# Performance work log

Measured on AMD Instinct MI355X. Metric: run time of the kernel, lower is better.

## Reference

```python
import jax, jax.numpy as jnp
import numpy as np

NEG_SLOPE = 0.2


def gatv2(x, src, dst, eattr, Wl, bl, Wr, br, We, att, bias, concat):
    # GATv2Conv (PyG semantics): message j->i, softmax over incoming edges of target i.
    n = x.shape[0]
    H, C = att.shape
    xl = (x @ Wl + bl).reshape(n, H, C)   # source transform lin_l
    xr = (x @ Wr + br).reshape(n, H, C)   # target transform lin_r
    xe = (eattr @ We).reshape(-1, H, C)   # edge transform lin_edge (no bias)
    g = jax.nn.leaky_relu(xl[src] + xr[dst] + xe, NEG_SLOPE)  # [E,H,C]
    e = jnp.einsum('ehc,hc->eh', g, att)                      # [E,H]
    m = jax.ops.segment_max(e, dst, num_segments=n)
    a = jnp.exp(e - m[dst])
    s = jax.ops.segment_sum(a, dst, num_segments=n)
    alpha = a / (s[dst] + 1e-16)                              # [E,H]
    out = jax.ops.segment_sum(alpha[:, :, None] * xl[src], dst, num_segments=n)
    out = out.reshape(n, H * C) if concat else out.mean(axis=1)
    return out + bias, alpha


def add_self_loops(src, dst, eattr, n):
    # PyG default: add_self_loops=True, fill_value='mean' for edge_attr
    loop = jnp.arange(n, dtype=src.dtype)
    fill = jnp.broadcast_to(eattr.mean(axis=0, keepdims=True), (n, eattr.shape[1]))
    return (jnp.concatenate([src, loop]), jnp.concatenate([dst, loop]),
            jnp.concatenate([eattr, fill], axis=0))


def setup_inputs() -> dict:
    key = jax.random.key(0)
    ks = iter(jax.random.split(key, 64))
    B, N, D = 4, 2048, 256
    n = B * N
    E = 131072
    H, C1 = 4, 64  # conv1: heads=4, out=hidden//heads=64 (concat -> 256)
    C2 = 256       # conv2: heads=4, out=256, concat=False (mean)
    IN1 = 770

    def rn(shape, s=0.05):
        return jax.random.normal(next(ks), shape, dtype=jnp.float32) * s

    inp = {
        'h': rn((B, N, D), 1.0), 'c_temp': rn((B, N, D), 1.0),
        'c_stereo': rn((B, N, D), 1.0), 'e_proj': rn((B, N, 2), 1.0),
        'f_Lt': rn((B, N, D), 1.0),
        'edges': jax.random.randint(next(ks), (2, E), 0, n, dtype=jnp.int64),
        'edge_attr': rn((E, 1), 1.0),
        # conv1
        'Wl1': rn((IN1, H * C1)), 'bl1': jnp.zeros((H * C1,), jnp.float32),
        'Wr1': rn((IN1, H * C1)), 'br1': jnp.zeros((H * C1,), jnp.float32),
        'We1': rn((1, H * C1)), 'att1': rn((H, C1)),
        'bias1': jnp.zeros((H * C1,), jnp.float32),
        # conv2
        'Wl2': rn((D, H * C2)), 'bl2': jnp.zeros((H * C2,), jnp.float32),
        'Wr2': rn((D, H * C2)), 'br2': jnp.zeros((H * C2,), jnp.float32),
        'We2': rn((1, H * C2)), 'att2': rn((H, C2)),
        'bias2': jnp.zeros((C2,), jnp.float32),
        # GRUCell ([in, 3H] layout; gate order r,z,n as in torch)
        'Wih': rn((D, 3 * D)), 'bih': jnp.zeros((3 * D,), jnp.float32),
        'Whh': rn((D, 3 * D)), 'bhh': jnp.zeros((3 * D,), jnp.float32),
        # heads
        'rW1': rn((D, 256)), 'rb1': jnp.zeros((256,), jnp.float32),
        'rW2': rn((256, 2)), 'rb2': jnp.zeros((2,), jnp.float32),
        'wW1': rn((D, 256)), 'wb1': jnp.zeros((256,), jnp.float32),
        'wW2': rn((256, 2)), 'wb2': jnp.zeros((2,), jnp.float32),
        'pW1': rn((D, 128)), 'pb1': jnp.zeros((128,), jnp.float32),
        'pW2': rn((128, 1)), 'pb2': jnp.zeros((1,), jnp.float32),
        'dW1': rn((D, 128)), 'db1': jnp.zeros((128,), jnp.float32),
        'dW2': rn((128, 1)), 'db2': jnp.zeros((1,), jnp.float32),
    }
    return inp


def reference(h, c_temp, c_stereo, e_proj, f_Lt, edges, edge_attr,
              Wl1, bl1, Wr1, br1, We1, att1, bias1,
              Wl2, bl2, Wr2, br2, We2, att2, bias2,
              Wih, bih, Whh, bhh,
              rW1, rb1, rW2, rb2, wW1, wb1, wW2, wb2,
              pW1, pb1, pW2, pb2, dW1, db1, dW2, db2):
    B, N, D = f_Lt.shape
    n = B * N
    x = jnp.concatenate([c_temp, c_stereo, e_proj, f_Lt], axis=-1).reshape(n, -1)

    src, dst, ea = add_self_loops(edges[0], edges[1], edge_attr, n)
    x1, _ = gatv2(x, src, dst, ea, Wl1, bl1, Wr1, br1, We1, att1, bias1, concat=True)
    x1 = jax.nn.relu(x1)
    x2, alpha = gatv2(x1, src, dst, ea, Wl2, bl2, Wr2, br2, We2, att2, bias2, concat=False)

    # GRUCell
    hf = h.reshape(n, -1)
    gi = x2 @ Wih + bih
    gh = hf @ Whh + bhh
    ir, iz, inew = jnp.split(gi, 3, axis=-1)
    hr, hz, hnew = jnp.split(gh, 3, axis=-1)
    r_g = jax.nn.sigmoid(ir + hr)
    z_g = jax.nn.sigmoid(iz + hz)
    n_g = jnp.tanh(inew + r_g * hnew)
    h_new = ((1.0 - z_g) * n_g + z_g * hf).reshape(B, N, D)

    res = jax.nn.relu(h_new @ rW1 + rb1) @ rW2 + rb2
    w = jax.nn.sigmoid(jax.nn.relu(h_new @ wW1 + wb1) @ wW2 + wb2)
    a_p = jax.nn.softplus(jax.nn.relu(h_new @ pW1 + pb1) @ pW2 + pb2).mean(axis=1)
    a_d = jax.nn.softplus(jax.nn.relu(h_new @ dW1 + db1) @ dW2 + db2)
    return (h_new, res, w, a_p, a_d)
```

## Files before the change

### kernel.cpp

```cpp
#include <hip/hip_runtime.h>
#include <hip/hip_bf16.h>
#include <cstdint>
#include <cstddef>

#define N_NODES 8192
#define E_RAW   131072
#define E_TOT   (E_RAW + N_NODES)
#define HEADS   4

typedef __attribute__((ext_vector_type(8))) __bf16 bf16x8;
typedef __attribute__((ext_vector_type(4))) float f32x4;
typedef __attribute__((ext_vector_type(2))) float f32x2;

__device__ __forceinline__ void gload_lds16(const void* g, void* lds) {
  __builtin_amdgcn_global_load_lds(
      (const __attribute__((address_space(1))) unsigned int*)g,
      (__attribute__((address_space(3))) unsigned int*)lds, 16, 0, 0);
}

__device__ __forceinline__ float bfbits2f(unsigned short u) {
  return __uint_as_float((unsigned)u << 16);
}
__device__ __forceinline__ unsigned short f2bfbits(float f) {
  __hip_bfloat16 b = __float2bfloat16(f);
  return *(unsigned short*)&b;
}
__device__ __forceinline__ f32x2 unpk2(unsigned u) {
  return (f32x2){__uint_as_float(u << 16), __uint_as_float(u & 0xffff0000u)};
}

__device__ __forceinline__ int eSrc(const int* __restrict__ src, int e) {
  return (e < E_RAW) ? src[e] : (e - E_RAW);
}
__device__ __forceinline__ int eDst(const int* __restrict__ dst, int e) {
  return (e < E_RAW) ? dst[e] : (e - E_RAW);
}


__global__ __launch_bounds__(256) void prep_kernel(
    const float* __restrict__ ct, const float* __restrict__ cs,
    const float* __restrict__ ep, const float* __restrict__ fl,
    const float* __restrict__ h, const float* __restrict__ ea,
    const float* bl1, const float* br1, const float* bl2, const float* br2,
    const float* rb1, const float* wb1, const float* pb1, const float* db1,
    __hip_bfloat16* __restrict__ x, __hip_bfloat16* __restrict__ Hb,
    float* __restrict__ MP, int* __restrict__ icnt_ipos,
    float* B1, float* B2, float* BH) {
  int blk = blockIdx.x;
  int tid = threadIdx.x;
  if (blk < 8192) {
    int i = blk;
    for (int j = tid; j < 832; j += 256) {
      float v;
      if (j < 256)      v = ct[(size_t)i * 256 + j];
      else if (j < 512) v = cs[(size_t)i * 256 + (j - 256)];
      else if (j < 514) v = ep[(size_t)i * 2 + (j - 512)];
      else if (j < 770) v = fl[(size_t)i * 256 + (j - 514)];
      else              v = 0.f;
      x[(size_t)i * 832 + j] = __float2bfloat16(v);
    }
  } else if (blk < 9216) {
    size_t base = ((size_t)(blk - 8192) * 256 + tid) * 8;
    float4 a = *(const float4*)(h + base);
    float4 b = *(const float4*)(h + base + 4);
    unsigned short o[8];
    o[0]=f2bfbits(a.x); o[1]=f2bfbits(a.y); o[2]=f2bfbits(a.z); o[3]=f2bfbits(a.w);
    o[4]=f2bfbits(b.x); o[5]=f2bfbits(b.y); o[6]=f2bfbits(b.z); o[7]=f2bfbits(b.w);
    *(uint4*)((unsigned short*)Hb + base) = *(uint4*)o;
  } else if (blk < 9472) {
    __shared__ float sm[256];
    int bb = blk - 9216;
    float acc = 0.f;
    for (int i = bb * 256 + tid; i < E_RAW; i += 256 * 256) acc += ea[i];
    sm[tid] = acc; __syncthreads();
    for (int s = 128; s; s >>= 1) { if (tid < s) sm[tid] += sm[tid + s]; __syncthreads(); }
    if (tid == 0) MP[bb] = sm[0];
  } else if (blk < 9536) {
    int i = (blk - 9472) * 256 + tid;
    if (i < 2 * N_NODES) icnt_ipos[i] = 0;
  } else {
    int i = (blk - 9536) * 256 + tid;
    if (i < 512) B1[i] = (i < 256) ? bl1[i] : br1[i - 256];
    else if (i < 2560) { int k = i - 512; B2[k] = (k < 1024) ? bl2[k] : br2[k - 1024]; }
    else if (i < 3328) {
      int k = i - 2560;
      BH[k] = (k < 256) ? rb1[k] : (k < 512) ? wb1[k - 256] : (k < 640) ? pb1[k - 512] : db1[k - 640];
    }
  }
}


__global__ void csr_count(const int* __restrict__ dst, int* __restrict__ cnt) {
  int e = blockIdx.x * blockDim.x + threadIdx.x;
  if (e < E_TOT) atomicAdd(&cnt[eDst(dst, e)], 1);
}

__global__ __launch_bounds__(1024) void csr_scan(const int* __restrict__ cnt,
                                                 int* __restrict__ off,
                                                 float* __restrict__ MP) {
  __shared__ int part[1024];
  __shared__ float sm[256];
  int t = threadIdx.x;
  if (t < 256) sm[t] = MP[t];
  __syncthreads();
  for (int s = 128; s; s >>= 1) { if (t < s) sm[t] += sm[t + s]; __syncthreads(); }
  if (t == 0) MP[256] = sm[0] * (1.f / (float)E_RAW);
  int base = t * 8;
  int loc[8];
  int s = 0;
#pragma unroll
  for (int i = 0; i < 8; ++i) { loc[i] = s; s += cnt[base + i]; }
  part[t] = s; __syncthreads();
  for (int d = 1; d < 1024; d <<= 1) {
    int v = (t >= d) ? part[t - d] : 0;
    __syncthreads();
    part[t] += v;
    __syncthreads();
  }
  int pre = (t == 0) ? 0 : part[t - 1];
#pragma unroll
  for (int i = 0; i < 8; ++i) off[base + i] = pre + loc[i];
  if (t == 1023) off[8192] = part[1023];
}

__global__ void csr_fill(const int* __restrict__ src, const int* __restrict__ dst,
                         const float* __restrict__ ea, const float* __restrict__ eamean,
                         const int* __restrict__ off, int* __restrict__ pos,
                         int* __restrict__ srcn, float* __restrict__ eav) {
  int e = blockIdx.x * blockDim.x + threadIdx.x;
  if (e >= E_TOT) return;
  int d = eDst(dst, e);
  int p = off[d] + atomicAdd(&pos[d], 1);
  srcn[p] = eSrc(src, e);
  eav[p] = (e < E_RAW) ? ea[e] : eamean[0];
}


__global__ __launch_bounds__(256) void wt_all(
    const float* w0, const float* w1, const float* w2, const float* w3,
    const float* w4, const float* w5, const float* w6, const float* w7,
    const float* w8, const float* w9,
    __hip_bfloat16* WT1, __hip_bfloat16* WT2, __hip_bfloat16* WTih,
    __hip_bfloat16* WThh, __hip_bfloat16* WTh) {
  const int cum[10] = {208, 416, 672, 928, 1120, 1312, 1376, 1440, 1472, 1504};
  const int Kt[10]  = {770, 770, 256, 256, 256, 256, 256, 256, 256, 256};
  const int Nt[10]  = {256, 256, 1024, 1024, 768, 768, 256, 256, 128, 128};
  const int KPt[10] = {832, 832, 256, 256, 256, 256, 256, 256, 256, 256};
  const int n0t[10] = {0, 256, 0, 1024, 0, 0, 0, 256, 512, 640};
  int job = 0;
  while (blockIdx.x >= (unsigned)cum[job]) ++job;
  int lb = blockIdx.x - (job ? cum[job - 1] : 0);
  int K = Kt[job], N = Nt[job], KP = KPt[job], n0 = n0t[job];
  int tilesX = KP >> 5;
  int k0 = (lb % tilesX) * 32, nb = (lb / tilesX) * 32;
  const float* W;
  switch (job) {
    case 0: W = w0; break; case 1: W = w1; break; case 2: W = w2; break;
    case 3: W = w3; break; case 4: W = w4; break; case 5: W = w5; break;
    case 6: W = w6; break; case 7: W = w7; break; case 8: W = w8; break;
    default: W = w9; break;
  }
  __hip_bfloat16* WT = (job < 2) ? WT1 : (job < 4) ? WT2 : (job == 4) ? WTih
                       : (job == 5) ? WThh : WTh;
  __shared__ float sm[32][33];
  int tx = threadIdx.x & 31, ty = threadIdx.x >> 5;
  for (int yy = ty; yy < 32; yy += 8) {
    int k = k0 + yy, n = nb + tx;
    sm[yy][tx] = (k < K && n < N) ? W[(size_t)k * N + n] : 0.f;
  }
  __syncthreads();
  for (int yy = ty; yy < 32; yy += 8) {
    int n = nb + yy, k = k0 + tx;
    if (n < N) WT[(size_t)(n0 + n) * KP + k] = __float2bfloat16(sm[tx][yy]);
  }
}


template <int OUT>
__global__ __launch_bounds__(512) void mfma_gemm(
    const __hip_bfloat16* __restrict__ A, const __hip_bfloat16* __restrict__ BT,
    const float* __restrict__ bias, void* __restrict__ Cout, int KP, int N,
    const __hip_bfloat16* A2, const __hip_bfloat16* BT2,
    const float* bias2, void* C2) {
  if (blockIdx.z == 1) { A = A2; BT = BT2; bias = bias2; Cout = C2; }
  __shared__ uint4 AsBuf[1024];
  __shared__ uint4 BsBuf[1024];
  char* Asc = (char*)AsBuf;
  char* Bsc = (char*)BsBuf;
  int tid = threadIdx.x;
  int lane = tid & 63;
  int wid = tid >> 6;
  int wr = wid >> 1;
  int wc = wid & 1;
  int bm = blockIdx.y * 128;
  int bn = blockIdx.x * 128;
  f32x4 acc[2][4];
#pragma unroll
  for (int i = 0; i < 2; ++i)
#pragma unroll
    for (int j = 0; j < 4; ++j) acc[i][j] = (f32x4){0.f, 0.f, 0.f, 0.f};

  int nK = KP >> 6;
  for (int kt = 0; kt < nK; ++kt) {
    int k0 = kt * 64;
#pragma unroll
    for (int i = 0; i < 2; ++i) {
      int p = i * 512 + tid;
      int row = p >> 3, cc = p & 7;
      int sc = cc ^ (row & 7);
      gload_lds16(A + (size_t)(bm + row) * KP + k0 + sc * 8, Asc + p * 16);
      gload_lds16(BT + (size_t)(bn + row) * KP + k0 + sc * 8, Bsc + p * 16);
    }
    __syncthreads();
#pragma unroll
    for (int s = 0; s < 2; ++s) {
      bf16x8 af[2], bfr[4];
#pragma unroll
      for (int f = 0; f < 2; ++f) {
        int r = wr * 32 + f * 16 + (lane & 15);
        int ch = (s * 4 + (lane >> 4)) ^ (r & 7);
        af[f] = *(const bf16x8*)(Asc + r * 128 + ch * 16);
      }
#pragma unroll
      for (int f = 0; f < 4; ++f) {
        int n = wc * 64 + f * 16 + (lane & 15);
        int cb = (s * 4 + (lane >> 4)) ^ (n & 7);
        bfr[f] = *(const bf16x8*)(Bsc + n * 128 + cb * 16);
      }
#pragma unroll
      for (int fm = 0; fm < 2; ++fm)
#pragma unroll
        for (int fn = 0; fn < 4; ++fn)
          acc[fm][fn] = __builtin_amdgcn_mfma_f32_16x16x32_bf16(af[fm], bfr[fn], acc[fm][fn], 0, 0, 0);
    }
    __syncthreads();
  }
  int rbase = bm + wr * 32 + (lane >> 4) * 4;
  int cbase = bn + wc * 64 + (lane & 15);
#pragma unroll
  for (int fm = 0; fm < 2; ++fm)
#pragma unroll
    for (int fn = 0; fn < 4; ++fn) {
      int col = cbase + fn * 16;
      float bv = bias[col];
#pragma unroll
      for (int j = 0; j < 4; ++j) {
        int row = rbase + fm * 16 + j;
        float v = acc[fm][fn][j] + bv;
        if (OUT == 2 || OUT == 3) v = fmaxf(v, 0.f);
        if (OUT == 0 || OUT == 3)
          ((__hip_bfloat16*)Cout)[(size_t)row * N + col] = __float2bfloat16(v);
        else
          ((float*)Cout)[(size_t)row * N + col] = v;
      }
    }
}


__global__ __launch_bounds__(256) void gat_fused1(
    const __hip_bfloat16* __restrict__ XLR,
    const int* __restrict__ off, const int* __restrict__ srcn,
    const float* __restrict__ eav, const float* __restrict__ We,
    const float* __restrict__ att, const float* __restrict__ bias,
    __hip_bfloat16* __restrict__ X1) {
  int d = (blockIdx.x * 256 + threadIdx.x) >> 6;
  int lane = threadIdx.x & 63;
  int q = lane & 15;
  int j0 = (lane >> 4) * 64 + q * 4;
  const unsigned short* X = (const unsigned short*)XLR;
  uint2 xv = *(const uint2*)(X + (size_t)d * 512 + 256 + j0);
  f32x2 xr[2] = {unpk2(xv.x), unpk2(xv.y)};
  f32x2 we[2] = {*(const f32x2*)(We + j0), *(const f32x2*)(We + j0 + 2)};
  f32x2 at[2] = {*(const f32x2*)(att + j0), *(const f32x2*)(att + j0 + 2)};
  int b = off[d], e1 = off[d + 1], pe = e1 - 1;
  int sB = srcn[b]; float eaA = eav[b];
  uint2 vA = *(const uint2*)(X + (size_t)sB * 512 + j0);
  int p1 = min(b + 1, pe); sB = srcn[p1]; float eaB = eav[p1];
  float m = -INFINITY, ss = 0.f;
  f32x2 a[2] = {(f32x2){0.f, 0.f}, (f32x2){0.f, 0.f}};
  for (int p = b; p < e1; ++p) {
    uint2 vu = vA; float ea = eaA; eaA = eaB;
    vA = *(const uint2*)(X + (size_t)sB * 512 + j0);
    int p2 = min(p + 2, pe); sB = srcn[p2]; eaB = eav[p2];
    f32x2 v[2] = {unpk2(vu.x), unpk2(vu.y)};
    f32x2 ea2 = (f32x2){ea, ea};
    f32x2 t2 = (f32x2){0.f, 0.f};
#pragma unroll
    for (int i = 0; i < 2; ++i) {
      f32x2 gg = (v[i] + xr[i]) + ea2 * we[i];
      f32x2 lr = __builtin_elementwise_max(gg, 0.2f * gg);
      t2 = t2 + lr * at[i];
    }
    float t = t2.x + t2.y;
    t += __shfl_xor(t, 8, 64); t += __shfl_xor(t, 4, 64);
    t += __shfl_xor(t, 2, 64); t += __shfl_xor(t, 1, 64);
    if (__all(t <= m)) {
      float wp = __expf(t - m);
      ss += wp;
      f32x2 wp2 = (f32x2){wp, wp};
#pragma unroll
      for (int i = 0; i < 2; ++i) a[i] = a[i] + wp2 * v[i];
    } else {
      float mn = fmaxf(m, t);
      float scl = __expf(m - mn);
      float wp = __expf(t - mn);
      ss = fmaf(ss, scl, wp);
      f32x2 wp2 = (f32x2){wp, wp}, s2 = (f32x2){scl, scl};
#pragma unroll
      for (int i = 0; i < 2; ++i) a[i] = a[i] * s2 + wp2 * v[i];
      m = mn;
    }
  }
  float inv = 1.f / (ss + 1e-16f);
  unsigned short o[4];
  o[0] = f2bfbits(fmaxf(fmaf(a[0].x, inv, bias[j0]), 0.f));
  o[1] = f2bfbits(fmaxf(fmaf(a[0].y, inv, bias[j0 + 1]), 0.f));
  o[2] = f2bfbits(fmaxf(fmaf(a[1].x, inv, bias[j0 + 2]), 0.f));
  o[3] = f2bfbits(fmaxf(fmaf(a[1].y, inv, bias[j0 + 3]), 0.f));
  *(uint2*)((unsigned short*)X1 + (size_t)d * 256 + j0) = *(uint2*)o;
}


__global__ __launch_bounds__(256) void gat_fused2(
    const __hip_bfloat16* __restrict__ XLR,
    const int* __restrict__ off, const int* __restrict__ srcn,
    const float* __restrict__ eav, const float* __restrict__ We,
    const float* __restrict__ att, const float* __restrict__ bias,
    __hip_bfloat16* __restrict__ X2) {
  int d = (blockIdx.x * 256 + threadIdx.x) >> 6;
  int lane = threadIdx.x & 63;
  int g = lane >> 4, q = lane & 15;
  int j0 = g * 256 + q * 16;
  const unsigned short* X = (const unsigned short*)XLR;
  f32x2 xr[8], we[8], at[8], a[8];
  {
    const uint4* xp = (const uint4*)(X + (size_t)d * 2048 + 1024 + j0);
    uint4 r0 = xp[0], r1 = xp[1];
    xr[0] = unpk2(r0.x); xr[1] = unpk2(r0.y); xr[2] = unpk2(r0.z); xr[3] = unpk2(r0.w);
    xr[4] = unpk2(r1.x); xr[5] = unpk2(r1.y); xr[6] = unpk2(r1.z); xr[7] = unpk2(r1.w);
#pragma unroll
    for (int i = 0; i < 8; ++i) {
      we[i] = *(const f32x2*)(We + j0 + 2 * i);
      at[i] = *(const f32x2*)(att + j0 + 2 * i);
      a[i] = (f32x2){0.f, 0.f};
    }
  }
  int b = off[d], e1 = off[d + 1], pe = e1 - 1;
  int sB = srcn[b]; float eaA = eav[b];
  const uint4* rp = (const uint4*)(X + (size_t)sB * 2048 + j0);
  uint4 rA0 = rp[0], rA1 = rp[1];
  int p1 = min(b + 1, pe); sB = srcn[p1]; float eaB = eav[p1];
  float m = -INFINITY, ss = 0.f;
  for (int p = b; p < e1; ++p) {
    uint4 c0 = rA0, c1 = rA1; float ea = eaA; eaA = eaB;
    rp = (const uint4*)(X + (size_t)sB * 2048 + j0);
    rA0 = rp[0]; rA1 = rp[1];
    int p2 = min(p + 2, pe); sB = srcn[p2]; eaB = eav[p2];
    f32x2 v[8];
    v[0] = unpk2(c0.x); v[1] = unpk2(c0.y); v[2] = unpk2(c0.z); v[3] = unpk2(c0.w);
    v[4] = unpk2(c1.x); v[5] = unpk2(c1.y); v[6] = unpk2(c1.z); v[7] = unpk2(c1.w);
    f32x2 ea2 = (f32x2){ea, ea};
    f32x2 t2 = (f32x2){0.f, 0.f};
#pragma unroll
    for (int i = 0; i < 8; ++i) {
      f32x2 gg = (v[i] + xr[i]) + ea2 * we[i];
      f32x2 lr = __builtin_elementwise_max(gg, 0.2f * gg);
      t2 = t2 + lr * at[i];
    }
    float t = t2.x + t2.y;
    t += __shfl_xor(t, 8, 64); t += __shfl_xor(t, 4, 64);
    t += __shfl_xor(t, 2, 64); t += __shfl_xor(t, 1, 64);
    if (__all(t <= m)) {
      float wp = __expf(t - m);
      ss += wp;
      f32x2 wp2 = (f32x2){wp, wp};
#pragma unroll
      for (int i = 0; i < 8; ++i) a[i] = a[i] + wp2 * v[i];
    } else {
      float mn = fmaxf(m, t);
      float scl = __expf(m - mn);
      float wp = __expf(t - mn);
      ss = fmaf(ss, scl, wp);
      f32x2 wp2 = (f32x2){wp, wp}, s2 = (f32x2){scl, scl};
#pragma unroll
      for (int i = 0; i < 8; ++i) a[i] = a[i] * s2 + wp2 * v[i];
      m = mn;
    }
  }
  float inv = 1.f / (ss + 1e-16f);
  f32x2 inv2 = (f32x2){inv, inv};
#pragma unroll
  for (int i = 0; i < 8; ++i) {
    f32x2 r2 = a[i] * inv2;
    r2.x += __shfl_xor(r2.x, 16, 64);
    r2.x += __shfl_xor(r2.x, 32, 64);
    r2.y += __shfl_xor(r2.y, 16, 64);
    r2.y += __shfl_xor(r2.y, 32, 64);
    a[i] = r2;
  }
  if (g == 0) {
    unsigned short o[16];
#pragma unroll
    for (int i = 0; i < 8; ++i) {
      o[2 * i]     = f2bfbits(fmaf(0.25f, a[i].x, bias[q * 16 + 2 * i]));
      o[2 * i + 1] = f2bfbits(fmaf(0.25f, a[i].y, bias[q * 16 + 2 * i + 1]));
    }
    uint4* op = (uint4*)((unsigned short*)X2 + (size_t)d * 256 + q * 16);
    op[0] = ((uint4*)o)[0];
    op[1] = ((uint4*)o)[1];
  }
}


__global__ void gru_kernel(const __hip_bfloat16* __restrict__ gi,
                           const __hip_bfloat16* __restrict__ gh,
                           const float* __restrict__ hf, float* __restrict__ hn,
                           __hip_bfloat16* __restrict__ hnb) {
  int i = blockIdx.x;
  int c = threadIdx.x;
  size_t b = (size_t)i * 768;
  const unsigned short* giu = (const unsigned short*)gi;
  const unsigned short* ghu = (const unsigned short*)gh;
  float ir = bfbits2f(giu[b + c]), iz = bfbits2f(giu[b + 256 + c]), in_ = bfbits2f(giu[b + 512 + c]);
  float hr = bfbits2f(ghu[b + c]), hz = bfbits2f(ghu[b + 256 + c]), hn_ = bfbits2f(ghu[b + 512 + c]);
  float r = 1.f / (1.f + __expf(-(ir + hr)));
  float z = 1.f / (1.f + __expf(-(iz + hz)));
  float ng = tanhf(in_ + r * hn_);
  float h0 = hf[(size_t)i * 256 + c];
  float v = (1.f - z) * ng + z * h0;
  hn[(size_t)i * 256 + c] = v;
  hnb[(size_t)i * 256 + c] = __float2bfloat16(v);
}


__global__ __launch_bounds__(256) void heads_final(
    const __hip_bfloat16* __restrict__ Tb,
    const float* __restrict__ rW2, const float* __restrict__ rb2,
    const float* __restrict__ wW2, const float* __restrict__ wb2,
    const float* __restrict__ pW2, const float* __restrict__ pb2,
    const float* __restrict__ dW2, const float* __restrict__ db2,
    float* __restrict__ o_res, float* __restrict__ o_w,
    float* __restrict__ AP, float* __restrict__ o_ad) {
  int node = (blockIdx.x * 256 + threadIdx.x) >> 6;
  int lane = threadIdx.x & 63;
  const unsigned short* t = (const unsigned short*)Tb + (size_t)node * 768;
  ushort4 tr = *(const ushort4*)(t + lane * 4);
  ushort4 tw = *(const ushort4*)(t + 256 + lane * 4);
  float trf[4] = {bfbits2f(tr.x), bfbits2f(tr.y), bfbits2f(tr.z), bfbits2f(tr.w)};
  float twf[4] = {bfbits2f(tw.x), bfbits2f(tw.y), bfbits2f(tw.z), bfbits2f(tw.w)};
  float tpf[4] = {0.f, 0.f, 0.f, 0.f}, tdf[4] = {0.f, 0.f, 0.f, 0.f};
  if (lane < 32) {
    ushort4 tp = *(const ushort4*)(t + 512 + lane * 4);
    ushort4 td = *(const ushort4*)(t + 640 + lane * 4);
    tpf[0] = bfbits2f(tp.x); tpf[1] = bfbits2f(tp.y); tpf[2] = bfbits2f(tp.z); tpf[3] = bfbits2f(tp.w);
    tdf[0] = bfbits2f(td.x); tdf[1] = bfbits2f(td.y); tdf[2] = bfbits2f(td.z); tdf[3] = bfbits2f(td.w);
  }
  float r0 = 0.f, r1 = 0.f, w0 = 0.f, w1 = 0.f, pp = 0.f, dd = 0.f;
#pragma unroll
  for (int i = 0; i < 4; ++i) {
    int k = lane * 4 + i;
    r0 = fmaf(trf[i], rW2[k * 2], r0);
    r1 = fmaf(trf[i], rW2[k * 2 + 1], r1);
    w0 = fmaf(twf[i], wW2[k * 2], w0);
    w1 = fmaf(twf[i], wW2[k * 2 + 1], w1);
  }
  if (lane < 32) {
#pragma unroll
    for (int i = 0; i < 4; ++i) {
      int k = lane * 4 + i;
      pp = fmaf(tpf[i], pW2[k], pp);
      dd = fmaf(tdf[i], dW2[k], dd);
    }
  }
#pragma unroll
  for (int o = 32; o; o >>= 1) {
    r0 += __shfl_xor(r0, o, 64); r1 += __shfl_xor(r1, o, 64);
    w0 += __shfl_xor(w0, o, 64); w1 += __shfl_xor(w1, o, 64);
    pp += __shfl_xor(pp, o, 64); dd += __shfl_xor(dd, o, 64);
  }
  if (lane == 0) {
    o_res[(size_t)node * 2]     = r0 + rb2[0];
    o_res[(size_t)node * 2 + 1] = r1 + rb2[1];
    float sw0 = w0 + wb2[0], sw1 = w1 + wb2[1];
    o_w[(size_t)node * 2]     = 1.f / (1.f + __expf(-sw0));
    o_w[(size_t)node * 2 + 1] = 1.f / (1.f + __expf(-sw1));
    float vp = pp + pb2[0];
    AP[node] = fmaxf(vp, 0.f) + log1pf(__expf(-fabsf(vp)));
    float vd = dd + db2[0];
    o_ad[node] = fmaxf(vd, 0.f) + log1pf(__expf(-fabsf(vd)));
  }
}

__global__ void ap_reduce(const float* __restrict__ ap, float* __restrict__ out) {
  __shared__ float sm[256];
  int b = blockIdx.x, tid = threadIdx.x;
  float acc = 0.f;
  for (int i = tid; i < 2048; i += 256) acc += ap[b * 2048 + i];
  sm[tid] = acc; __syncthreads();
  for (int s = 128; s; s >>= 1) { if (tid < s) sm[tid] += sm[tid + s]; __syncthreads(); }
  if (tid == 0) out[b] = sm[0] * (1.f / 2048.f);
}


extern "C" void kernel_launch(void* const* d_in, const int* in_sizes, int n_in,
                              void* d_out, int out_size, void* d_ws, size_t ws_size,
                              hipStream_t stream) {
  const float* h        = (const float*)d_in[0];
  const float* c_temp   = (const float*)d_in[1];
  const float* c_stereo = (const float*)d_in[2];
  const float* e_proj   = (const float*)d_in[3];
  const float* f_Lt     = (const float*)d_in[4];
  const int*   edges    = (const int*)d_in[5];
  const float* eattr    = (const float*)d_in[6];
  const float* Wl1 = (const float*)d_in[7];  const float* bl1 = (const float*)d_in[8];
  const float* Wr1 = (const float*)d_in[9];  const float* br1 = (const float*)d_in[10];
  const float* We1 = (const float*)d_in[11]; const float* att1 = (const float*)d_in[12];
  const float* bias1 = (const float*)d_in[13];
  const float* Wl2 = (const float*)d_in[14]; const float* bl2 = (const float*)d_in[15];
  const float* Wr2 = (const float*)d_in[16]; const float* br2 = (const float*)d_in[17];
  const float* We2 = (const float*)d_in[18]; const float* att2 = (const float*)d_in[19];
  const float* bias2 = (const float*)d_in[20];
  const float* Wih = (const float*)d_in[21]; const float* bih = (const float*)d_in[22];
  const float* Whh = (const float*)d_in[23]; const float* bhh = (const float*)d_in[24];
  const float* rW1 = (const float*)d_in[25]; const float* rb1 = (const float*)d_in[26];
  const float* rW2 = (const float*)d_in[27]; const float* rb2 = (const float*)d_in[28];
  const float* wW1 = (const float*)d_in[29]; const float* wb1 = (const float*)d_in[30];
  const float* wW2 = (const float*)d_in[31]; const float* wb2 = (const float*)d_in[32];
  const float* pW1 = (const float*)d_in[33]; const float* pb1 = (const float*)d_in[34];
  const float* pW2 = (const float*)d_in[35]; const float* pb2 = (const float*)d_in[36];
  const float* dW1 = (const float*)d_in[37]; const float* db1 = (const float*)d_in[38];
  const float* dW2 = (const float*)d_in[39]; const float* db2 = (const float*)d_in[40];

  const int* src = edges;
  const int* dst = edges + E_RAW;

  float* base = (float*)d_ws;
  size_t cur = 0;
  auto alloc = [&](size_t n) { float* p = base + cur; cur += (n + 63) & ~(size_t)63; return p; };

  float* BIG0 = alloc(8388608);
  float* BIG1 = alloc(6291456);
  float* XLR1f = alloc(2097152);
  float* X1f  = alloc(1048576);
  float* X2f  = alloc(1048576);
  float* Hbf  = alloc(1048576);
  float* HNbf = alloc(1048576);
  float* WT1f = alloc(212992);
  float* WT2f = alloc(262144);
  float* WTihf = alloc(98304);
  float* WThhf = alloc(98304);
  float* WThf  = alloc(98304);
  float* B1 = alloc(512);
  float* B2 = alloc(2048);
  float* BH = alloc(768);
  float* EAV = alloc(E_TOT);
  float* AP  = alloc(N_NODES);
  float* MP  = alloc(320);
  int* ICNT = (int*)alloc(2 * N_NODES);
  int* IOFF = (int*)alloc(N_NODES + 64);
  int* ISRC = (int*)alloc(E_TOT);
  if (ws_size < cur * 4) return;
  int* IPOS = ICNT + N_NODES;

  __hip_bfloat16* x_bf = (__hip_bfloat16*)BIG1;
  __hip_bfloat16* XLR1 = (__hip_bfloat16*)XLR1f;
  __hip_bfloat16* XLR2 = (__hip_bfloat16*)BIG0;
  __hip_bfloat16* X1b = (__hip_bfloat16*)X1f;
  __hip_bfloat16* X2b = (__hip_bfloat16*)X2f;
  __hip_bfloat16* Hb  = (__hip_bfloat16*)Hbf;
  __hip_bfloat16* HNb = (__hip_bfloat16*)HNbf;
  __hip_bfloat16* WT1 = (__hip_bfloat16*)WT1f;
  __hip_bfloat16* WT2 = (__hip_bfloat16*)WT2f;
  __hip_bfloat16* WTih = (__hip_bfloat16*)WTihf;
  __hip_bfloat16* WThh = (__hip_bfloat16*)WThhf;
  __hip_bfloat16* WTh  = (__hip_bfloat16*)WThf;
  __hip_bfloat16* gi = (__hip_bfloat16*)BIG0;
  __hip_bfloat16* gh = (__hip_bfloat16*)BIG1;
  __hip_bfloat16* Tb = (__hip_bfloat16*)BIG0;

  float* o_hnew = (float*)d_out;
  float* o_res  = o_hnew + (size_t)N_NODES * 256;
  float* o_w    = o_res + (size_t)N_NODES * 2;
  float* o_ap   = o_w + (size_t)N_NODES * 2;
  float* o_ad   = o_ap + 4;

  prep_kernel<<<9549, 256, 0, stream>>>(c_temp, c_stereo, e_proj, f_Lt, h, eattr,
                                        bl1, br1, bl2, br2, rb1, wb1, pb1, db1,
                                        x_bf, Hb, MP, ICNT, B1, B2, BH);
  csr_count<<<(E_TOT + 255) / 256, 256, 0, stream>>>(dst, ICNT);
  csr_scan<<<1, 1024, 0, stream>>>(ICNT, IOFF, MP);
  csr_fill<<<(E_TOT + 255) / 256, 256, 0, stream>>>(src, dst, eattr, MP + 256,
                                                    IOFF, IPOS, ISRC, EAV);
  wt_all<<<1504, 256, 0, stream>>>(Wl1, Wr1, Wl2, Wr2, Wih, Whh, rW1, wW1, pW1, dW1,
                                   WT1, WT2, WTih, WThh, WTh);

  mfma_gemm<0><<<dim3(4, 64, 1), 512, 0, stream>>>(x_bf, WT1, B1, XLR1, 832, 512,
                                                   nullptr, nullptr, nullptr, nullptr);
  gat_fused1<<<N_NODES / 4, 256, 0, stream>>>(XLR1, IOFF, ISRC, EAV, We1, att1, bias1, X1b);

  mfma_gemm<0><<<dim3(16, 64, 1), 512, 0, stream>>>(X1b, WT2, B2, XLR2, 256, 2048,
                                                    nullptr, nullptr, nullptr, nullptr);
  gat_fused2<<<N_NODES / 4, 256, 0, stream>>>(XLR2, IOFF, ISRC, EAV, We2, att2, bias2, X2b);

  mfma_gemm<0><<<dim3(6, 64, 2), 512, 0, stream>>>(X2b, WTih, bih, gi, 256, 768,
                                                   Hb, WThh, bhh, gh);
  gru_kernel<<<N_NODES, 256, 0, stream>>>(gi, gh, h, o_hnew, HNb);

  mfma_gemm<3><<<dim3(6, 64, 1), 512, 0, stream>>>(HNb, WTh, BH, Tb, 256, 768,
                                                   nullptr, nullptr, nullptr, nullptr);
  heads_final<<<N_NODES / 4, 256, 0, stream>>>(Tb, rW2, rb2, wW2, wb2, pW2, pb2, dW2, db2,
                                               o_res, o_w, AP, o_ad);
  ap_reduce<<<4, 256, 0, stream>>>(AP, o_ap);
}
```

Before: 209.0 us.

## Sort destination nodes by in-degree for balanced GAT aggregation waves

Builds a degree histogram during the CSR scan and a new perm_fill kernel that orders nodes by descending in-degree, so the two GAT aggregation kernels visit destinations through this permutation. Wavefronts in the same block then process nodes with similar edge counts, which is meant to cut the divergence and tail imbalance that random degrees cause. The kernels also drop from two-deep to one-deep prefetch and gain an occupancy hint of 8 blocks per SM to lower register pressure. The cost is one extra small kernel launch and less latency hiding per wave.

```diff
diff --git a/kernel.cpp b/kernel.cpp
--- a/kernel.cpp
+++ b/kernel.cpp
@@ -45,7 +45,7 @@
     const float* rb1, const float* wb1, const float* pb1, const float* db1,
     __hip_bfloat16* __restrict__ x, __hip_bfloat16* __restrict__ Hb,
     float* __restrict__ MP, int* __restrict__ icnt_ipos,
-    float* B1, float* B2, float* BH) {
+    float* B1, float* B2, float* BH, int* __restrict__ dpos) {
   int blk = blockIdx.x;
   int tid = threadIdx.x;
   if (blk < 8192) {
@@ -85,6 +85,8 @@
     else if (i < 3328) {
       int k = i - 2560;
       BH[k] = (k < 256) ? rb1[k] : (k < 512) ? wb1[k - 256] : (k < 640) ? pb1[k - 512] : db1[k - 640];
+    } else if (i < 3392) {
+      dpos[i - 3328] = 0;
     }
   }
 }
@@ -97,20 +99,27 @@
 
 __global__ __launch_bounds__(1024) void csr_scan(const int* __restrict__ cnt,
                                                  int* __restrict__ off,
-                                                 float* __restrict__ MP) {
+                                                 float* __restrict__ MP,
+                                                 int* __restrict__ doff) {
   __shared__ int part[1024];
   __shared__ float sm[256];
+  __shared__ int hist[64];
   int t = threadIdx.x;
   if (t < 256) sm[t] = MP[t];
+  if (t < 64) hist[t] = 0;
   __syncthreads();
   for (int s = 128; s; s >>= 1) { if (t < s) sm[t] += sm[t + s]; __syncthreads(); }
   if (t == 0) MP[256] = sm[0] * (1.f / (float)E_RAW);
   int base = t * 8;
   int loc[8];
-  int s = 0;
-#pragma unroll
-  for (int i = 0; i < 8; ++i) { loc[i] = s; s += cnt[base + i]; }
-  part[t] = s; __syncthreads();
+  int acc8 = 0;
+#pragma unroll
+  for (int i = 0; i < 8; ++i) {
+    int c = cnt[base + i];
+    loc[i] = acc8; acc8 += c;
+    atomicAdd(&hist[min(c, 63)], 1);
+  }
+  part[t] = acc8; __syncthreads();
   for (int d = 1; d < 1024; d <<= 1) {
     int v = (t >= d) ? part[t - d] : 0;
     __syncthreads();
@@ -121,6 +130,11 @@
 #pragma unroll
   for (int i = 0; i < 8; ++i) off[base + i] = pre + loc[i];
   if (t == 1023) off[8192] = part[1023];
+  __syncthreads();
+  if (t == 0) {
+    int acc = 0;
+    for (int bb = 63; bb >= 0; --bb) { doff[bb] = acc; acc += hist[bb]; }
+  }
 }
 
 __global__ void csr_fill(const int* __restrict__ src, const int* __restrict__ dst,
@@ -133,6 +147,15 @@
   int p = off[d] + atomicAdd(&pos[d], 1);
   srcn[p] = eSrc(src, e);
   eav[p] = (e < E_RAW) ? ea[e] : eamean[0];
+}
+
+__global__ void perm_fill(const int* __restrict__ cnt, const int* __restrict__ doff,
+                          int* __restrict__ dpos, int* __restrict__ perm) {
+  int i = blockIdx.x * 256 + threadIdx.x;
+  if (i >= N_NODES) return;
+  int bin = min(cnt[i], 63);
+  int pos = doff[bin] + atomicAdd(&dpos[bin], 1);
+  perm[pos] = i;
 }
 
 
@@ -257,13 +280,13 @@
 }
 
 
-__global__ __launch_bounds__(256) void gat_fused1(
+__global__ __launch_bounds__(256, 8) void gat_fused1(
     const __hip_bfloat16* __restrict__ XLR,
     const int* __restrict__ off, const int* __restrict__ srcn,
-    const float* __restrict__ eav, const float* __restrict__ We,
-    const float* __restrict__ att, const float* __restrict__ bias,
-    __hip_bfloat16* __restrict__ X1) {
-  int d = (blockIdx.x * 256 + threadIdx.x) >> 6;
+    const float* __restrict__ eav, const int* __restrict__ perm,
+    const float* __restrict__ We, const float* __restrict__ att,
+    const float* __restrict__ bias, __hip_bfloat16* __restrict__ X1) {
+  int d = perm[(blockIdx.x * 256 + threadIdx.x) >> 6];
   int lane = threadIdx.x & 63;
   int q = lane & 15;
   int j0 = (lane >> 4) * 64 + q * 4;
@@ -273,15 +296,14 @@
   f32x2 we[2] = {*(const f32x2*)(We + j0), *(const f32x2*)(We + j0 + 2)};
   f32x2 at[2] = {*(const f32x2*)(att + j0), *(const f32x2*)(att + j0 + 2)};
   int b = off[d], e1 = off[d + 1], pe = e1 - 1;
-  int sB = srcn[b]; float eaA = eav[b];
-  uint2 vA = *(const uint2*)(X + (size_t)sB * 512 + j0);
-  int p1 = min(b + 1, pe); sB = srcn[p1]; float eaB = eav[p1];
+  int sA = srcn[b]; float eaA = eav[b];
   float m = -INFINITY, ss = 0.f;
   f32x2 a[2] = {(f32x2){0.f, 0.f}, (f32x2){0.f, 0.f}};
   for (int p = b; p < e1; ++p) {
-    uint2 vu = vA; float ea = eaA; eaA = eaB;
-    vA = *(const uint2*)(X + (size_t)sB * 512 + j0);
-    int p2 = min(p + 2, pe); sB = srcn[p2]; eaB = eav[p2];
+    uint2 vu = *(const uint2*)(X + (size_t)sA * 512 + j0);
+    float ea = eaA;
+    int pn = min(p + 1, pe);
+    sA = srcn[pn]; eaA = eav[pn];
     f32x2 v[2] = {unpk2(vu.x), unpk2(vu.y)};
     f32x2 ea2 = (f32x2){ea, ea};
     f32x2 t2 = (f32x2){0.f, 0.f};
@@ -321,13 +343,13 @@
 }
 
 
-__global__ __launch_bounds__(256) void gat_fused2(
+__global__ __launch_bounds__(256, 8) void gat_fused2(
     const __hip_bfloat16* __restrict__ XLR,
     const int* __restrict__ off, const int* __restrict__ srcn,
-    const float* __restrict__ eav, const float* __restrict__ We,
-    const float* __restrict__ att, const float* __restrict__ bias,
-    __hip_bfloat16* __restrict__ X2) {
-  int d = (blockIdx.x * 256 + threadIdx.x) >> 6;
+    const float* __restrict__ eav, const int* __restrict__ perm,
+    const float* __restrict__ We, const float* __restrict__ att,
+    const float* __restrict__ bias, __hip_bfloat16* __restrict__ X2) {
+  int d = perm[(blockIdx.x * 256 + threadIdx.x) >> 6];
   int lane = threadIdx.x & 63;
   int g = lane >> 4, q = lane & 15;
   int j0 = g * 256 + q * 16;
@@ -346,16 +368,14 @@
     }
   }
   int b = off[d], e1 = off[d + 1], pe = e1 - 1;
-  int sB = srcn[b]; float eaA = eav[b];
-  const uint4* rp = (const uint4*)(X + (size_t)sB * 2048 + j0);
-  uint4 rA0 = rp[0], rA1 = rp[1];
-  int p1 = min(b + 1, pe); sB = srcn[p1]; float eaB = eav[p1];
+  int sA = srcn[b]; float eaA = eav[b];
   float m = -INFINITY, ss = 0.f;
   for (int p = b; p < e1; ++p) {
-    uint4 c0 = rA0, c1 = rA1; float ea = eaA; eaA = eaB;
-    rp = (const uint4*)(X + (size_t)sB * 2048 + j0);
-    rA0 = rp[0]; rA1 = rp[1];
-    int p2 = min(p + 2, pe); sB = srcn[p2]; eaB = eav[p2];
+    const uint4* rp = (const uint4*)(X + (size_t)sA * 2048 + j0);
+    uint4 c0 = rp[0], c1 = rp[1];
+    float ea = eaA;
+    int pn = min(p + 1, pe);
+    sA = srcn[pn]; eaA = eav[pn];
     f32x2 v[8];
     v[0] = unpk2(c0.x); v[1] = unpk2(c0.y); v[2] = unpk2(c0.z); v[3] = unpk2(c0.w);
     v[4] = unpk2(c1.x); v[5] = unpk2(c1.y); v[6] = unpk2(c1.z); v[7] = unpk2(c1.w);
@@ -559,6 +579,9 @@
   int* ICNT = (int*)alloc(2 * N_NODES);
   int* IOFF = (int*)alloc(N_NODES + 64);
   int* ISRC = (int*)alloc(E_TOT);
+  int* DOFF = (int*)alloc(64);
+  int* DPOS = (int*)alloc(64);
+  int* PERM = (int*)alloc(N_NODES);
   if (ws_size < cur * 4) return;
   int* IPOS = ICNT + N_NODES;
 
@@ -584,23 +607,24 @@
   float* o_ap   = o_w + (size_t)N_NODES * 2;
   float* o_ad   = o_ap + 4;
 
-  prep_kernel<<<9549, 256, 0, stream>>>(c_temp, c_stereo, e_proj, f_Lt, h, eattr,
+  prep_kernel<<<9550, 256, 0, stream>>>(c_temp, c_stereo, e_proj, f_Lt, h, eattr,
                                         bl1, br1, bl2, br2, rb1, wb1, pb1, db1,
-                                        x_bf, Hb, MP, ICNT, B1, B2, BH);
+                                        x_bf, Hb, MP, ICNT, B1, B2, BH, DPOS);
   csr_count<<<(E_TOT + 255) / 256, 256, 0, stream>>>(dst, ICNT);
-  csr_scan<<<1, 1024, 0, stream>>>(ICNT, IOFF, MP);
+  csr_scan<<<1, 1024, 0, stream>>>(ICNT, IOFF, MP, DOFF);
   csr_fill<<<(E_TOT + 255) / 256, 256, 0, stream>>>(src, dst, eattr, MP + 256,
                                                     IOFF, IPOS, ISRC, EAV);
+  perm_fill<<<(N_NODES + 255) / 256, 256, 0, stream>>>(ICNT, DOFF, DPOS, PERM);
   wt_all<<<1504, 256, 0, stream>>>(Wl1, Wr1, Wl2, Wr2, Wih, Whh, rW1, wW1, pW1, dW1,
                                    WT1, WT2, WTih, WThh, WTh);
 
   mfma_gemm<0><<<dim3(4, 64, 1), 512, 0, stream>>>(x_bf, WT1, B1, XLR1, 832, 512,
                                                    nullptr, nullptr, nullptr, nullptr);
-  gat_fused1<<<N_NODES / 4, 256, 0, stream>>>(XLR1, IOFF, ISRC, EAV, We1, att1, bias1, X1b);
+  gat_fused1<<<N_NODES / 4, 256, 0, stream>>>(XLR1, IOFF, ISRC, EAV, PERM, We1, att1, bias1, X1b);
 
   mfma_gemm<0><<<dim3(16, 64, 1), 512, 0, stream>>>(X1b, WT2, B2, XLR2, 256, 2048,
                                                     nullptr, nullptr, nullptr, nullptr);
-  gat_fused2<<<N_NODES / 4, 256, 0, stream>>>(XLR2, IOFF, ISRC, EAV, We2, att2, bias2, X2b);
+  gat_fused2<<<N_NODES / 4, 256, 0, stream>>>(XLR2, IOFF, ISRC, EAV, PERM, We2, att2, bias2, X2b);
 
   mfma_gemm<0><<<dim3(6, 64, 2), 512, 0, stream>>>(X2b, WTih, bih, gi, 256, 768,
                                                    Hb, WThh, bhh, gh);
```

After: 511.7 us. +144.9%, slower.

## Split gat_fused2 heads across two wavefronts per node and reduce via LDS

Applied to the files above, without the earlier changes.

The second GATv2 aggregation kernel now assigns each node to two wavefronts, each covering two heads with 8 channels per lane, instead of one wavefront covering all four heads with 16 channels per lane. The cross-head mean is done through shared memory after a block barrier rather than with lane shuffles. The grid doubles to N/2 blocks of 2 nodes each. Gather prefetch depth is cut from two edges ahead to one, and the per-lane register footprint shrinks. This is meant to raise parallelism and occupancy for the latency-bound gather, at the cost of an extra shuffle step, an LDS round trip, a barrier, and less prefetching.

```diff
diff --git a/kernel.cpp b/kernel.cpp
--- a/kernel.cpp
+++ b/kernel.cpp
@@ -327,87 +327,77 @@
     const float* __restrict__ eav, const float* __restrict__ We,
     const float* __restrict__ att, const float* __restrict__ bias,
     __hip_bfloat16* __restrict__ X2) {
-  int d = (blockIdx.x * 256 + threadIdx.x) >> 6;
-  int lane = threadIdx.x & 63;
-  int g = lane >> 4, q = lane & 15;
-  int j0 = g * 256 + q * 16;
+  __shared__ float lds_a[2][4][256];
+  int tid = threadIdx.x;
+  int w = tid >> 6;
+  int nl = w >> 1;
+  int wp = w & 1;
+  int lane = tid & 63;
+  int hh = lane >> 5;
+  int head = wp * 2 + hh;
+  int l5 = lane & 31;
+  int d = blockIdx.x * 2 + nl;
+  int j0 = head * 256 + l5 * 8;
   const unsigned short* X = (const unsigned short*)XLR;
-  f32x2 xr[8], we[8], at[8], a[8];
-  {
-    const uint4* xp = (const uint4*)(X + (size_t)d * 2048 + 1024 + j0);
-    uint4 r0 = xp[0], r1 = xp[1];
-    xr[0] = unpk2(r0.x); xr[1] = unpk2(r0.y); xr[2] = unpk2(r0.z); xr[3] = unpk2(r0.w);
-    xr[4] = unpk2(r1.x); xr[5] = unpk2(r1.y); xr[6] = unpk2(r1.z); xr[7] = unpk2(r1.w);
-#pragma unroll
-    for (int i = 0; i < 8; ++i) {
-      we[i] = *(const f32x2*)(We + j0 + 2 * i);
-      at[i] = *(const f32x2*)(att + j0 + 2 * i);
-      a[i] = (f32x2){0.f, 0.f};
-    }
+  uint4 xv = *(const uint4*)(X + (size_t)d * 2048 + 1024 + j0);
+  f32x2 xr[4] = {unpk2(xv.x), unpk2(xv.y), unpk2(xv.z), unpk2(xv.w)};
+  f32x2 we[4], at[4], a[4];
+#pragma unroll
+  for (int i = 0; i < 4; ++i) {
+    we[i] = *(const f32x2*)(We + j0 + 2 * i);
+    at[i] = *(const f32x2*)(att + j0 + 2 * i);
+    a[i] = (f32x2){0.f, 0.f};
   }
   int b = off[d], e1 = off[d + 1], pe = e1 - 1;
-  int sB = srcn[b]; float eaA = eav[b];
-  const uint4* rp = (const uint4*)(X + (size_t)sB * 2048 + j0);
-  uint4 rA0 = rp[0], rA1 = rp[1];
-  int p1 = min(b + 1, pe); sB = srcn[p1]; float eaB = eav[p1];
+  int sA = srcn[b]; float eaA = eav[b];
   float m = -INFINITY, ss = 0.f;
   for (int p = b; p < e1; ++p) {
-    uint4 c0 = rA0, c1 = rA1; float ea = eaA; eaA = eaB;
-    rp = (const uint4*)(X + (size_t)sB * 2048 + j0);
-    rA0 = rp[0]; rA1 = rp[1];
-    int p2 = min(p + 2, pe); sB = srcn[p2]; eaB = eav[p2];
-    f32x2 v[8];
-    v[0] = unpk2(c0.x); v[1] = unpk2(c0.y); v[2] = unpk2(c0.z); v[3] = unpk2(c0.w);
-    v[4] = unpk2(c1.x); v[5] = unpk2(c1.y); v[6] = unpk2(c1.z); v[7] = unpk2(c1.w);
+    uint4 cc = *(const uint4*)(X + (size_t)sA * 2048 + j0);
+    float ea = eaA;
+    int pn = min(p + 1, pe);
+    sA = srcn[pn]; eaA = eav[pn];
+    f32x2 v[4] = {unpk2(cc.x), unpk2(cc.y), unpk2(cc.z), unpk2(cc.w)};
     f32x2 ea2 = (f32x2){ea, ea};
     f32x2 t2 = (f32x2){0.f, 0.f};
 #pragma unroll
-    for (int i = 0; i < 8; ++i) {
+    for (int i = 0; i < 4; ++i) {
       f32x2 gg = (v[i] + xr[i]) + ea2 * we[i];
       f32x2 lr = __builtin_elementwise_max(gg, 0.2f * gg);
       t2 = t2 + lr * at[i];
     }
     float t = t2.x + t2.y;
-    t += __shfl_xor(t, 8, 64); t += __shfl_xor(t, 4, 64);
-    t += __shfl_xor(t, 2, 64); t += __shfl_xor(t, 1, 64);
+    t += __shfl_xor(t, 16, 64); t += __shfl_xor(t, 8, 64);
+    t += __shfl_xor(t, 4, 64);  t += __shfl_xor(t, 2, 64);
+    t += __shfl_xor(t, 1, 64);
     if (__all(t <= m)) {
-      float wp = __expf(t - m);
-      ss += wp;
-      f32x2 wp2 = (f32x2){wp, wp};
-#pragma unroll
-      for (int i = 0; i < 8; ++i) a[i] = a[i] + wp2 * v[i];
+      float wv = __expf(t - m);
+      ss += wv;
+      f32x2 wv2 = (f32x2){wv, wv};
+#pragma unroll
+      for (int i = 0; i < 4; ++i) a[i] = a[i] + wv2 * v[i];
     } else {
       float mn = fmaxf(m, t);
       float scl = __expf(m - mn);
-      float wp = __expf(t - mn);
-      ss = fmaf(ss, scl, wp);
-      f32x2 wp2 = (f32x2){wp, wp}, s2 = (f32x2){scl, scl};
-#pragma unroll
-      for (int i = 0; i < 8; ++i) a[i] = a[i] * s2 + wp2 * v[i];
+      float wv = __expf(t - mn);
+      ss = fmaf(ss, scl, wv);
+      f32x2 wv2 = (f32x2){wv, wv}, s2 = (f32x2){scl, scl};
+#pragma unroll
+      for (int i = 0; i < 4; ++i) a[i] = a[i] * s2 + wv2 * v[i];
       m = mn;
     }
   }
   float inv = 1.f / (ss + 1e-16f);
-  f32x2 inv2 = (f32x2){inv, inv};
-#pragma unroll
-  for (int i = 0; i < 8; ++i) {
-    f32x2 r2 = a[i] * inv2;
-    r2.x += __shfl_xor(r2.x, 16, 64);
-    r2.x += __shfl_xor(r2.x, 32, 64);
-    r2.y += __shfl_xor(r2.y, 16, 64);
-    r2.y += __shfl_xor(r2.y, 32, 64);
-    a[i] = r2;
-  }
-  if (g == 0) {
-    unsigned short o[16];
-#pragma unroll
-    for (int i = 0; i < 8; ++i) {
-      o[2 * i]     = f2bfbits(fmaf(0.25f, a[i].x, bias[q * 16 + 2 * i]));
-      o[2 * i + 1] = f2bfbits(fmaf(0.25f, a[i].y, bias[q * 16 + 2 * i + 1]));
-    }
-    uint4* op = (uint4*)((unsigned short*)X2 + (size_t)d * 256 + q * 16);
-    op[0] = ((uint4*)o)[0];
-    op[1] = ((uint4*)o)[1];
+#pragma unroll
+  for (int i = 0; i < 4; ++i) {
+    f32x2 r2 = a[i] * (f32x2){inv, inv};
+    *(f32x2*)&lds_a[nl][head][l5 * 8 + 2 * i] = r2;
+  }
+  __syncthreads();
+  int c = tid & 255;
+#pragma unroll
+  for (int nn = 0; nn < 2; ++nn) {
+    float sv = lds_a[nn][0][c] + lds_a[nn][1][c] + lds_a[nn][2][c] + lds_a[nn][3][c];
+    X2[(size_t)(blockIdx.x * 2 + nn) * 256 + c] = __float2bfloat16(fmaf(0.25f, sv, bias[c]));
   }
 }
 
@@ -600,7 +590,7 @@
 
   mfma_gemm<0><<<dim3(16, 64, 1), 512, 0, stream>>>(X1b, WT2, B2, XLR2, 256, 2048,
                                                     nullptr, nullptr, nullptr, nullptr);
-  gat_fused2<<<N_NODES / 4, 256, 0, stream>>>(XLR2, IOFF, ISRC, EAV, We2, att2, bias2, X2b);
+  gat_fused2<<<N_NODES / 2, 256, 0, stream>>>(XLR2, IOFF, ISRC, EAV, We2, att2, bias2, X2b);
 
   mfma_gemm<0><<<dim3(6, 64, 2), 512, 0, stream>>>(X2b, WTih, bih, gi, 256, 768,
                                                    Hb, WThh, bhh, gh);
```

After: 214.0 us. +2.4%, slower.
